# Performance work log

Measured on AMD Instinct MI355X. Metric: run time of the kernel, lower is better.

## Reference

```python
import jax, jax.numpy as jnp
import numpy as np

RES = 7          # POOLER_RESOLUTION
SR = 2           # POOLER_SAMPLING_RATIO
SCALES = (0.25, 0.125, 0.0625, 0.03125)
CANONICAL_SCALE = 224.0
CANONICAL_LEVEL = 4.0
K_MIN, K_MAX = 2.0, 5.0  # -log2(SCALES[0]), -log2(SCALES[-1])


def setup_inputs() -> dict:
    key = jax.random.key(0)
    ks = jax.random.split(key, 9)
    feat0 = jax.random.normal(ks[0], (2, 256, 200, 200), dtype=jnp.float32)
    feat1 = jax.random.normal(ks[1], (2, 256, 100, 100), dtype=jnp.float32)
    feat2 = jax.random.normal(ks[2], (2, 256, 50, 50), dtype=jnp.float32)
    feat3 = jax.random.normal(ks[3], (2, 256, 25, 25), dtype=jnp.float32)
    R = 512
    x1 = jax.random.uniform(ks[4], (R,)) * 600.0
    y1 = jax.random.uniform(ks[5], (R,)) * 600.0
    w = 16.0 + jax.random.uniform(ks[6], (R,)) * 500.0
    h = 16.0 + jax.random.uniform(ks[7], (R,)) * 500.0
    boxes = jnp.stack([x1, y1, x1 + w, y1 + h], axis=1).astype(jnp.float32)
    batch_idx = jax.random.randint(ks[8], (R,), 0, 2, dtype=jnp.int32)
    return {"feat0": feat0, "feat1": feat1, "feat2": feat2, "feat3": feat3,
            "boxes": boxes, "batch_idx": batch_idx}


def _map_levels(boxes):
    # LevelMapper: floor(k0 + log2(sqrt(area)/224 + eps)), clamp to [k_min,k_max], shift
    area = jnp.maximum(boxes[:, 2] - boxes[:, 0], 0.0) * jnp.maximum(boxes[:, 3] - boxes[:, 1], 0.0)
    s = jnp.sqrt(area)
    lvl = jnp.floor(CANONICAL_LEVEL + jnp.log2(s / CANONICAL_SCALE + 1e-6))
    return (jnp.clip(lvl, K_MIN, K_MAX) - K_MIN).astype(jnp.int32)


def _roi_align(feat, boxes, batch_idx, scale):
    # feat: [B,C,H,W]; boxes: [R,4] (x1,y1,x2,y2) in image coords; ROIAlign (aligned=False)
    H, W = feat.shape[2], feat.shape[3]
    x1 = boxes[:, 0] * scale
    y1 = boxes[:, 1] * scale
    x2 = boxes[:, 2] * scale
    y2 = boxes[:, 3] * scale
    roi_w = jnp.maximum(x2 - x1, 1.0)
    roi_h = jnp.maximum(y2 - y1, 1.0)
    bin_w = roi_w / RES
    bin_h = roi_h / RES
    # sample-point offsets within the roi, in bin units: [RES*SR]
    p = (jnp.arange(RES, dtype=jnp.float32)[:, None]
         + (jnp.arange(SR, dtype=jnp.float32)[None, :] + 0.5) / SR).reshape(-1)
    ys = y1[:, None] + p[None, :] * bin_h[:, None]   # [R,S]
    xs = x1[:, None] + p[None, :] * bin_w[:, None]   # [R,S]
    valid_y = (ys >= -1.0) & (ys <= float(H))
    valid_x = (xs >= -1.0) & (xs <= float(W))
    yc = jnp.clip(ys, 0.0, float(H - 1))
    xc = jnp.clip(xs, 0.0, float(W - 1))
    y0 = jnp.floor(yc).astype(jnp.int32)
    x0 = jnp.floor(xc).astype(jnp.int32)
    y1i = jnp.minimum(y0 + 1, H - 1)
    x1i = jnp.minimum(x0 + 1, W - 1)
    ly = yc - y0.astype(jnp.float32)
    lx = xc - x0.astype(jnp.float32)
    hy = 1.0 - ly
    hx = 1.0 - lx
    b = batch_idx[:, None, None]  # [R,1,1]

    def gather(yi, xi):
        # advanced indexing -> [R,S,S,C]
        return feat[b, :, yi[:, :, None], xi[:, None, :]]

    v = (gather(y0, x0) * (hy[:, :, None] * hx[:, None, :])[..., None]
         + gather(y0, x1i) * (hy[:, :, None] * lx[:, None, :])[..., None]
         + gather(y1i, x0) * (ly[:, :, None] * hx[:, None, :])[..., None]
         + gather(y1i, x1i) * (ly[:, :, None] * lx[:, None, :])[..., None])
    v = v * (valid_y[:, :, None] & valid_x[:, None, :])[..., None].astype(v.dtype)
    R = boxes.shape[0]
    C = feat.shape[1]
    v = v.reshape(R, RES, SR, RES, SR, C).mean(axis=(2, 4))  # [R,RES,RES,C]
    return jnp.transpose(v, (0, 3, 1, 2))  # [R,C,RES,RES]


def reference(feat0, feat1, feat2, feat3, boxes, batch_idx):
    feats = (feat0, feat1, feat2, feat3)
    levels = _map_levels(boxes)
    out = jnp.zeros((boxes.shape[0], feat0.shape[1], RES, RES), dtype=feat0.dtype)
    for lvl, (f, sc) in enumerate(zip(feats, SCALES)):
        pooled = _roi_align(f, boxes, batch_idx, sc)
        out = out + jnp.where((levels == lvl)[:, None, None, None], pooled, 0.0)
    return out
```

## Files before the change

### kernel.cpp

```cpp
#include <hip/hip_runtime.h>
#include <hip/hip_bf16.h>

#define RES 7
#define NCH 256

__device__ __forceinline__ unsigned short f32_to_bf16_rne(float f) {
    unsigned int u = __float_as_uint(f);
    u += 0x7fffu + ((u >> 16) & 1u);
    return (unsigned short)(u >> 16);
}

__device__ __forceinline__ unsigned int pack_bf16x2(float lo, float hi) {
    return (unsigned int)f32_to_bf16_rne(lo) | ((unsigned int)f32_to_bf16_rne(hi) << 16);
}

__global__ __launch_bounds__(512) void transpose_dma_bf16(
    const float* __restrict__ f0, const float* __restrict__ f1,
    const float* __restrict__ f2, const float* __restrict__ f3,
    unsigned short* __restrict__ ws)
{
    __shared__ float ldsf[32 * 260];

    const int xt = blockIdx.x;
    const int cy = blockIdx.y;
    const int b  = blockIdx.z;

    const int l    = (xt >= 313) + (xt >= 392) + (xt >= 412);
    const int base = (l == 0) ? 0 : (l == 1) ? 313 : (l == 2) ? 392 : 412;
    const int HW   = (l == 0) ? 40000 : (l == 1) ? 10000 : (l == 2) ? 2500 : 625;
    const float* __restrict__ src =
        (l == 0) ? f0 : (l == 1) ? f1 : (l == 2) ? f2 : f3;
    const size_t doff = (l == 0) ? 0u : (l == 1) ? 20480000u
                      : (l == 2) ? 25600000u : 26880000u;

    const int hw0 = (xt - base) * 128;
    const int c0b = 64 * cy;

    const float* __restrict__ s    = src + (size_t)b * NCH * HW;
    unsigned short* __restrict__ d = ws + doff + (size_t)b * HW * NCH;

    const int t  = threadIdx.x;
    const int w  = t >> 6;
    const int ln = t & 63;

    const bool dma = (hw0 + 128 <= HW) && ((HW & 3) == 0);

    if (dma) {
#pragma unroll
        for (int q = 0; q < 4; ++q) {
            const int g = w * 4 + q;
            const int c = c0b + 2 * g + (ln >> 5);
            const float* gp = s + (size_t)c * HW + hw0 + (ln & 31) * 4;
            float* lp = &ldsf[g * 260];
            __builtin_amdgcn_global_load_lds(
                (const __attribute__((address_space(1))) void*)gp,
                (__attribute__((address_space(3))) void*)lp,
                16, 0, 0);
        }
    } else {
        const int hq  = t & 31;
        const int cr  = t >> 5;
        const int hwq = hw0 + 4 * hq;
        float va[4][4];
#pragma unroll
        for (int i = 0; i < 4; ++i)
#pragma unroll
            for (int j = 0; j < 4; ++j)
                va[i][j] = (hwq + j < HW)
                         ? s[(size_t)(c0b + 4 * cr + i) * HW + hwq + j] : 0.0f;
#pragma unroll
        for (int i = 0; i < 4; ++i) {
            const int c = 4 * cr + i;
#pragma unroll
            for (int j = 0; j < 4; ++j)
                ldsf[(c >> 1) * 260 + (c & 1) * 128 + 4 * hq + j] = va[i][j];
        }
    }
    __syncthreads();

#pragma unroll
    for (int it = 0; it < 4; ++it) {
        const int idx = t + 512 * it;
        const int row = idx >> 4;
        const int u   = idx & 15;
        const int hw  = hw0 + row;
        if (hw < HW) {
            const float v0 = ldsf[(2 * u) * 260 + row];
            const float v1 = ldsf[(2 * u) * 260 + 128 + row];
            const float v2 = ldsf[(2 * u + 1) * 260 + row];
            const float v3 = ldsf[(2 * u + 1) * 260 + 128 + row];
            uint2 p;
            p.x = pack_bf16x2(v0, v1);
            p.y = pack_bf16x2(v2, v3);
            *(uint2*)(d + (size_t)hw * NCH + c0b + 4 * u) = p;
        }
    }
}

__global__ __launch_bounds__(512) void roi_gather_nhwc_bf16(
    const unsigned short* __restrict__ ws,
    const float* __restrict__ boxes, const int* __restrict__ bidx,
    float* __restrict__ out)
{
    __shared__ float lds[49 * 260];

    const int r   = blockIdx.x;
    const int t   = threadIdx.x;
    const int cq  = t & 63;
    const int grp = t >> 6;

    const float bx1 = boxes[r * 4 + 0];
    const float by1 = boxes[r * 4 + 1];
    const float bx2 = boxes[r * 4 + 2];
    const float by2 = boxes[r * 4 + 3];

    const float area = fmaxf(bx2 - bx1, 0.0f) * fmaxf(by2 - by1, 0.0f);
    const float s    = sqrtf(area);
    const float lvlf = floorf(4.0f + log2f(s / 224.0f + 1e-6f));
    const int   lvl  = (int)(fminf(fmaxf(lvlf, 2.0f), 5.0f)) - 2;

    float scale; int H; size_t off;
    if      (lvl == 0) { scale = 0.25f;    H = 200; off = 0u; }
    else if (lvl == 1) { scale = 0.125f;   H = 100; off = 20480000u; }
    else if (lvl == 2) { scale = 0.0625f;  H = 50;  off = 25600000u; }
    else               { scale = 0.03125f; H = 25;  off = 26880000u; }
    const int W = H;

    const int b = bidx[r];
    const unsigned short* __restrict__ feat = ws + off + (size_t)b * H * W * NCH;

    const float x1 = bx1 * scale;
    const float y1 = by1 * scale;
    const float roi_w = fmaxf(bx2 * scale - x1, 1.0f);
    const float roi_h = fmaxf(by2 * scale - y1, 1.0f);
    const float bw = roi_w * (1.0f / RES);
    const float bh = roi_h * (1.0f / RES);

    for (int bin = grp; bin < 49; bin += 8) {
        const int py = bin / 7;
        const int px = bin - py * 7;

        float acc0 = 0.0f, acc1 = 0.0f, acc2 = 0.0f, acc3 = 0.0f;
#pragma unroll
        for (int sy = 0; sy < 2; ++sy) {
            const float pyf = (float)py + ((float)sy + 0.5f) * 0.5f;
            const float ysmp = y1 + pyf * bh;
            const bool  vy   = (ysmp >= -1.0f) && (ysmp <= (float)H);
            const float ycl  = fminf(fmaxf(ysmp, 0.0f), (float)(H - 1));
            const int   y0   = (int)floorf(ycl);
            const int   y1i  = min(y0 + 1, H - 1);
            const float ly   = ycl - (float)y0;
            const float hy   = 1.0f - ly;
#pragma unroll
            for (int sx = 0; sx < 2; ++sx) {
                const float pxf = (float)px + ((float)sx + 0.5f) * 0.5f;
                const float xsmp = x1 + pxf * bw;
                const bool  vx   = (xsmp >= -1.0f) && (xsmp <= (float)W);
                const float xcl  = fminf(fmaxf(xsmp, 0.0f), (float)(W - 1));
                const int   x0   = (int)floorf(xcl);
                const int   x1i  = min(x0 + 1, W - 1);
                const float lx   = xcl - (float)x0;
                const float hx   = 1.0f - lx;

                const float m   = (vy && vx) ? 1.0f : 0.0f;
                const float w00 = m * hy * hx;
                const float w01 = m * hy * lx;
                const float w10 = m * ly * hx;
                const float w11 = m * ly * lx;

                const uint2 u00 = *(const uint2*)(feat + ((size_t)(y0  * W + x0 )) * NCH + 4 * cq);
                const uint2 u01 = *(const uint2*)(feat + ((size_t)(y0  * W + x1i)) * NCH + 4 * cq);
                const uint2 u10 = *(const uint2*)(feat + ((size_t)(y1i * W + x0 )) * NCH + 4 * cq);
                const uint2 u11 = *(const uint2*)(feat + ((size_t)(y1i * W + x1i)) * NCH + 4 * cq);

                acc0 += w00 * __uint_as_float(u00.x << 16)
                      + w01 * __uint_as_float(u01.x << 16)
                      + w10 * __uint_as_float(u10.x << 16)
                      + w11 * __uint_as_float(u11.x << 16);
                acc1 += w00 * __uint_as_float(u00.x & 0xffff0000u)
                      + w01 * __uint_as_float(u01.x & 0xffff0000u)
                      + w10 * __uint_as_float(u10.x & 0xffff0000u)
                      + w11 * __uint_as_float(u11.x & 0xffff0000u);
                acc2 += w00 * __uint_as_float(u00.y << 16)
                      + w01 * __uint_as_float(u01.y << 16)
                      + w10 * __uint_as_float(u10.y << 16)
                      + w11 * __uint_as_float(u11.y << 16);
                acc3 += w00 * __uint_as_float(u00.y & 0xffff0000u)
                      + w01 * __uint_as_float(u01.y & 0xffff0000u)
                      + w10 * __uint_as_float(u10.y & 0xffff0000u)
                      + w11 * __uint_as_float(u11.y & 0xffff0000u);
            }
        }
        float4* dst = (float4*)&lds[bin * 260 + 4 * cq];
        *dst = make_float4(acc0 * 0.25f, acc1 * 0.25f, acc2 * 0.25f, acc3 * 0.25f);
    }

    __syncthreads();

    float* __restrict__ o = out + (size_t)r * (NCH * 49);
    for (int i = t; i < NCH * 49; i += 512) {
        const int ch = i / 49;
        const int bn = i - ch * 49;
        o[i] = lds[bn * 260 + ch];
    }
}

__global__ __launch_bounds__(256) void roi_align_fpn_kernel(
    const float* __restrict__ f0, const float* __restrict__ f1,
    const float* __restrict__ f2, const float* __restrict__ f3,
    const float* __restrict__ boxes, const int* __restrict__ bidx,
    float* __restrict__ out)
{
    const int r   = blockIdx.x;
    const int bin = blockIdx.y;
    const int c   = threadIdx.x;
    const int py  = bin / RES;
    const int px  = bin - py * RES;

    const float bx1 = boxes[r * 4 + 0];
    const float by1 = boxes[r * 4 + 1];
    const float bx2 = boxes[r * 4 + 2];
    const float by2 = boxes[r * 4 + 3];

    const float area = fmaxf(bx2 - bx1, 0.0f) * fmaxf(by2 - by1, 0.0f);
    const float s    = sqrtf(area);
    const float lvlf = floorf(4.0f + log2f(s / 224.0f + 1e-6f));
    const int   lvl  = (int)(fminf(fmaxf(lvlf, 2.0f), 5.0f)) - 2;

    const float scales[4] = {0.25f, 0.125f, 0.0625f, 0.03125f};
    const int   Hs[4]     = {200, 100, 50, 25};
    const float* feats[4] = {f0, f1, f2, f3};

    const float scale = scales[lvl];
    const int   H     = Hs[lvl];
    const int   W     = H;
    const float* feat = feats[lvl];

    const int b = bidx[r];

    const float x1 = bx1 * scale;
    const float y1 = by1 * scale;
    const float roi_w = fmaxf(bx2 * scale - x1, 1.0f);
    const float roi_h = fmaxf(by2 * scale - y1, 1.0f);
    const float bw = roi_w * (1.0f / RES);
    const float bh = roi_h * (1.0f / RES);

    const float* __restrict__ fc = feat + (size_t)(b * NCH + c) * H * W;

    float acc = 0.0f;
#pragma unroll
    for (int sy = 0; sy < 2; ++sy) {
        const float pyf = (float)py + ((float)sy + 0.5f) * 0.5f;
        const float ys  = y1 + pyf * bh;
        const bool  vy  = (ys >= -1.0f) && (ys <= (float)H);
        const float ycl = fminf(fmaxf(ys, 0.0f), (float)(H - 1));
        const int   y0  = (int)floorf(ycl);
        const int   y1i = min(y0 + 1, H - 1);
        const float ly  = ycl - (float)y0;
        const float hy  = 1.0f - ly;
#pragma unroll
        for (int sx = 0; sx < 2; ++sx) {
            const float pxf = (float)px + ((float)sx + 0.5f) * 0.5f;
            const float xs  = x1 + pxf * bw;
            const bool  vx  = (xs >= -1.0f) && (xs <= (float)W);
            const float xcl = fminf(fmaxf(xs, 0.0f), (float)(W - 1));
            const int   x0  = (int)floorf(xcl);
            const int   x1i = min(x0 + 1, W - 1);
            const float lx  = xcl - (float)x0;
            const float hx  = 1.0f - lx;

            const float v00 = fc[y0  * W + x0 ];
            const float v01 = fc[y0  * W + x1i];
            const float v10 = fc[y1i * W + x0 ];
            const float v11 = fc[y1i * W + x1i];

            const float v = v00 * (hy * hx) + v01 * (hy * lx)
                          + v10 * (ly * hx) + v11 * (ly * lx);
            if (vy && vx) acc += v;
        }
    }

    out[((size_t)r * NCH + c) * (RES * RES) + bin] = acc * 0.25f;
}

extern "C" void kernel_launch(void* const* d_in, const int* in_sizes, int n_in,
                              void* d_out, int out_size, void* d_ws, size_t ws_size,
                              hipStream_t stream)
{
    const float* f0    = (const float*)d_in[0];
    const float* f1    = (const float*)d_in[1];
    const float* f2    = (const float*)d_in[2];
    const float* f3    = (const float*)d_in[3];
    const float* boxes = (const float*)d_in[4];
    const int*   bidx  = (const int*)d_in[5];
    float* out = (float*)d_out;

    const int R = in_sizes[4] / 4;

    const size_t need = 27200000ull * sizeof(unsigned short);

    if (ws_size >= need) {
        unsigned short* ws = (unsigned short*)d_ws;
        transpose_dma_bf16<<<dim3(417, 4, 2), dim3(512), 0, stream>>>(f0, f1, f2, f3, ws);
        roi_gather_nhwc_bf16<<<dim3(R), dim3(512), 0, stream>>>(ws, boxes, bidx, out);
    } else {
        dim3 grid(R, RES * RES);
        roi_align_fpn_kernel<<<grid, dim3(NCH), 0, stream>>>(f0, f1, f2, f3, boxes, bidx, out);
    }
}
```

Measured before the change: 51.01 us.

## Replace transpose grid with persistent double-buffered LDS pipeline over smaller tiles

```diff
diff --git a/kernel.cpp b/kernel.cpp
--- a/kernel.cpp
+++ b/kernel.cpp
@@ -3,6 +3,11 @@
 
 #define RES 7
 #define NCH 256
+
+#define TJOBS 6656
+#define TJOBS_PER_B 3328
+#define TJOBS_PER_CG 832
+#define TGRID 1024
 
 __device__ __forceinline__ unsigned short f32_to_bf16_rne(float f) {
     unsigned int u = __float_as_uint(f);
@@ -14,86 +19,116 @@
     return (unsigned int)f32_to_bf16_rne(lo) | ((unsigned int)f32_to_bf16_rne(hi) << 16);
 }
 
-__global__ __launch_bounds__(512) void transpose_dma_bf16(
-    const float* __restrict__ f0, const float* __restrict__ f1,
-    const float* __restrict__ f2, const float* __restrict__ f3,
-    unsigned short* __restrict__ ws)
-{
-    __shared__ float ldsf[32 * 260];
-
-    const int xt = blockIdx.x;
-    const int cy = blockIdx.y;
-    const int b  = blockIdx.z;
-
-    const int l    = (xt >= 313) + (xt >= 392) + (xt >= 412);
-    const int base = (l == 0) ? 0 : (l == 1) ? 313 : (l == 2) ? 392 : 412;
+struct JobP {
+    const float* s;
+    unsigned short* d;
+    int HW, hw0, c0b;
+    bool dma;
+};
+
+__device__ __forceinline__ JobP decode_job(
+    int j, const float* f0, const float* f1, const float* f2, const float* f3,
+    unsigned short* ws)
+{
+    JobP jp;
+    const int b   = (j >= TJOBS_PER_B) ? 1 : 0;
+    const int rem = j - b * TJOBS_PER_B;
+    const int cg  = rem / TJOBS_PER_CG;
+    const int xt  = rem - cg * TJOBS_PER_CG;
+    const int l    = (xt >= 625) + (xt >= 782) + (xt >= 822);
+    const int base = (l == 0) ? 0 : (l == 1) ? 625 : (l == 2) ? 782 : 822;
     const int HW   = (l == 0) ? 40000 : (l == 1) ? 10000 : (l == 2) ? 2500 : 625;
-    const float* __restrict__ src =
-        (l == 0) ? f0 : (l == 1) ? f1 : (l == 2) ? f2 : f3;
+    const float* src = (l == 0) ? f0 : (l == 1) ? f1 : (l == 2) ? f2 : f3;
     const size_t doff = (l == 0) ? 0u : (l == 1) ? 20480000u
                       : (l == 2) ? 25600000u : 26880000u;
-
-    const int hw0 = (xt - base) * 128;
-    const int c0b = 64 * cy;
-
-    const float* __restrict__ s    = src + (size_t)b * NCH * HW;
-    unsigned short* __restrict__ d = ws + doff + (size_t)b * HW * NCH;
-
-    const int t  = threadIdx.x;
-    const int w  = t >> 6;
-    const int ln = t & 63;
-
-    const bool dma = (hw0 + 128 <= HW) && ((HW & 3) == 0);
-
-    if (dma) {
-#pragma unroll
-        for (int q = 0; q < 4; ++q) {
-            const int g = w * 4 + q;
-            const int c = c0b + 2 * g + (ln >> 5);
-            const float* gp = s + (size_t)c * HW + hw0 + (ln & 31) * 4;
-            float* lp = &ldsf[g * 260];
+    jp.HW  = HW;
+    jp.hw0 = (xt - base) * 64;
+    jp.c0b = 64 * cg;
+    jp.s   = src + (size_t)b * NCH * HW;
+    jp.d   = ws + doff + (size_t)b * HW * NCH;
+    jp.dma = (jp.hw0 + 64 <= HW) && ((HW & 3) == 0);
+    return jp;
+}
+
+__device__ __forceinline__ void stage_job(const JobP jp, float* buf, int t)
+{
+    if (jp.dma) {
+        const int w  = t >> 6;
+        const int ln = t & 63;
+#pragma unroll
+        for (int q = 0; q < 2; ++q) {
+            const int g = 2 * w + q;
+            const int c = jp.c0b + 4 * g + (ln >> 4);
+            const float* gp = jp.s + (size_t)c * jp.HW + jp.hw0 + (ln & 15) * 4;
+            float* lp = buf + g * 260;
             __builtin_amdgcn_global_load_lds(
                 (const __attribute__((address_space(1))) void*)gp,
                 (__attribute__((address_space(3))) void*)lp,
                 16, 0, 0);
         }
     } else {
-        const int hq  = t & 31;
-        const int cr  = t >> 5;
-        const int hwq = hw0 + 4 * hq;
-        float va[4][4];
-#pragma unroll
-        for (int i = 0; i < 4; ++i)
-#pragma unroll
-            for (int j = 0; j < 4; ++j)
-                va[i][j] = (hwq + j < HW)
-                         ? s[(size_t)(c0b + 4 * cr + i) * HW + hwq + j] : 0.0f;
-#pragma unroll
-        for (int i = 0; i < 4; ++i) {
-            const int c = 4 * cr + i;
-#pragma unroll
-            for (int j = 0; j < 4; ++j)
-                ldsf[(c >> 1) * 260 + (c & 1) * 128 + 4 * hq + j] = va[i][j];
-        }
-    }
-    __syncthreads();
-
-#pragma unroll
-    for (int it = 0; it < 4; ++it) {
+        const int cl = t >> 3;
+        const int p0 = (t & 7) * 8;
+        const int c  = jp.c0b + cl;
+#pragma unroll
+        for (int i = 0; i < 8; ++i) {
+            const int hw = jp.hw0 + p0 + i;
+            buf[(cl >> 2) * 260 + (cl & 3) * 64 + p0 + i] =
+                (hw < jp.HW) ? jp.s[(size_t)c * jp.HW + hw] : 0.0f;
+        }
+    }
+}
+
+__device__ __forceinline__ void store_job(const JobP jp, const float* buf, int t)
+{
+#pragma unroll
+    for (int it = 0; it < 2; ++it) {
         const int idx = t + 512 * it;
         const int row = idx >> 4;
         const int u   = idx & 15;
-        const int hw  = hw0 + row;
-        if (hw < HW) {
-            const float v0 = ldsf[(2 * u) * 260 + row];
-            const float v1 = ldsf[(2 * u) * 260 + 128 + row];
-            const float v2 = ldsf[(2 * u + 1) * 260 + row];
-            const float v3 = ldsf[(2 * u + 1) * 260 + 128 + row];
+        const int hw  = jp.hw0 + row;
+        if (hw < jp.HW) {
+            const float v0 = buf[u * 260 +  0 + row];
+            const float v1 = buf[u * 260 + 64 + row];
+            const float v2 = buf[u * 260 + 128 + row];
+            const float v3 = buf[u * 260 + 192 + row];
             uint2 p;
             p.x = pack_bf16x2(v0, v1);
             p.y = pack_bf16x2(v2, v3);
-            *(uint2*)(d + (size_t)hw * NCH + c0b + 4 * u) = p;
-        }
+            *(uint2*)(jp.d + (size_t)hw * NCH + jp.c0b + 4 * u) = p;
+        }
+    }
+}
+
+__global__ __launch_bounds__(512) void transpose_pipe_bf16(
+    const float* __restrict__ f0, const float* __restrict__ f1,
+    const float* __restrict__ f2, const float* __restrict__ f3,
+    unsigned short* __restrict__ ws)
+{
+    __shared__ float ldsf[2 * 4160];
+
+    const int t = threadIdx.x;
+
+    int j = blockIdx.x;
+    JobP cur = decode_job(j, f0, f1, f2, f3, ws);
+    int curbuf = 0;
+    stage_job(cur, ldsf, t);
+
+    for (;;) {
+        const int nj = j + TGRID;
+        const bool has = (nj < TJOBS);
+        JobP nxt;
+        if (has) nxt = decode_job(nj, f0, f1, f2, f3, ws);
+
+        __syncthreads();
+
+        if (has) stage_job(nxt, ldsf + (curbuf ^ 1) * 4160, t);
+        store_job(cur, ldsf + curbuf * 4160, t);
+
+        if (!has) break;
+        cur = nxt;
+        j = nj;
+        curbuf ^= 1;
     }
 }
 
@@ -301,7 +336,7 @@
 
     if (ws_size >= need) {
         unsigned short* ws = (unsigned short*)d_ws;
-        transpose_dma_bf16<<<dim3(417, 4, 2), dim3(512), 0, stream>>>(f0, f1, f2, f3, ws);
+        transpose_pipe_bf16<<<dim3(TGRID), dim3(512), 0, stream>>>(f0, f1, f2, f3, ws);
         roi_gather_nhwc_bf16<<<dim3(R), dim3(512), 0, stream>>>(ws, boxes, bidx, out);
     } else {
         dim3 grid(R, RES * RES);
```

After: 53.70 us. 5.3% more time.
